# Kernel tuning notes

Hardware: AMD Instinct MI355X
Metric: run time of the kernel (lower is better)

## Reference

```python
import jax, jax.numpy as jnp
import numpy as np

MOMENTUM = 0.1
C_DIM = 5


def setup_inputs() -> dict:
    key = jax.random.key(0)
    k1, k2, k3 = jax.random.split(key, 3)
    B, C, H, W = 16, 256, 128, 128
    im = jax.random.normal(k1, (B, C, H, W), dtype=jnp.float32)
    running_mean = jnp.zeros((2 * C_DIM, C), dtype=jnp.float32)
    running_std = jnp.ones((2 * C_DIM, C), dtype=jnp.float32)
    c_trg = jax.random.randint(k2, (B, C_DIM), 0, 2, dtype=jnp.int32)
    c_org = jax.random.randint(k3, (B, C_DIM), 0, 2, dtype=jnp.int32)
    return {"im": im, "running_mean": running_mean, "running_std": running_std,
            "c_trg": c_trg, "c_org": c_org}


def reference(im, running_mean, running_std, c_trg, c_org):
    B, C, H, W = im.shape
    N = H * W
    # per-sample per-channel instance stats; torch.std_mean uses correction=1
    mean = jnp.mean(im, axis=(2, 3))                      # [B, C]
    var = jnp.sum((im - mean[:, :, None, None]) ** 2, axis=(2, 3)) / (N - 1)
    std = jnp.sqrt(var)                                   # [B, C]

    ct = c_trg.astype(bool)
    co = c_org.astype(bool)
    c_trg_full = jnp.concatenate([ct, ~ct], axis=1)       # [B, 2*c_dim]
    c_org_full = jnp.concatenate([co, ~co], axis=1)       # [B, 2*c_dim]

    m = jnp.float32(MOMENTUM)

    # sequential EMA update of running buffers, in batch order (matches torch loop)
    def step(carry, xs):
        rm, rs = carry
        std_n, mean_n, org_n = xs                         # [C], [C], [2*c_dim]
        msk = org_n[:, None]                              # [2*c_dim, 1]
        rs = jnp.where(msk, rs * (1 - m) + std_n[None, :] * m, rs)
        rm = jnp.where(msk, rm * (1 - m) + mean_n[None, :] * m, rm)
        return (rm, rs), None

    (rm_final, rs_final), _ = jax.lax.scan(
        step, (running_mean, running_std), (std, mean, c_org_full))

    # per-sample gather: mean of selected buffer rows. Exactly c_dim rows are
    # selected per sample (each attribute contributes itself or its negation).
    sel = c_trg_full.astype(im.dtype)                     # [B, 2*c_dim]
    cnt = jnp.sum(sel, axis=1, keepdims=True)             # [B, 1] (== c_dim)
    trg_std = (sel @ rs_final) / cnt                      # [B, C]
    trg_mean = (sel @ rm_final) / cnt                     # [B, C]

    def bc(x):  # [B, C] -> [B, C, 1, 1]
        return x[:, :, None, None]

    return (im - bc(mean)) / bc(std) * bc(trg_std) + bc(trg_mean)
```

## Files before the change

### kernel.cpp

```cpp
#include <hip/hip_runtime.h>
#include <math.h>

#define CDIM 5
constexpr int B_ = 16;
constexpr int C_ = 256;
constexpr int HW_ = 128 * 128;
constexpr float MOM = 0.1f;

using f32x4 = __attribute__((ext_vector_type(4))) float;

__global__ __launch_bounds__(256) void cin_stats(const float* __restrict__ im,
                                                 float* __restrict__ ws_mean,
                                                 float* __restrict__ ws_std) {
    const int plane = blockIdx.x;
    const f32x4* p4 = (const f32x4*)(im + (size_t)plane * HW_);
    const int t = threadIdx.x;

    float sum = 0.f, sumsq = 0.f;
    #pragma unroll
    for (int it = 0; it < 16; ++it) {
        f32x4 v = p4[it * 256 + t];
        sum   += v.x + v.y + v.z + v.w;
        sumsq += v.x * v.x + v.y * v.y + v.z * v.z + v.w * v.w;
    }

    #pragma unroll
    for (int off = 32; off > 0; off >>= 1) {
        sum   += __shfl_down(sum, off, 64);
        sumsq += __shfl_down(sumsq, off, 64);
    }

    __shared__ float s_sum[4], s_sq[4];
    const int wave = t >> 6;
    if ((t & 63) == 0) { s_sum[wave] = sum; s_sq[wave] = sumsq; }
    __syncthreads();

    if (t == 0) {
        float s = s_sum[0] + s_sum[1] + s_sum[2] + s_sum[3];
        float q = s_sq[0] + s_sq[1] + s_sq[2] + s_sq[3];
        float mean = s / (float)HW_;
        float var = fmaxf(q - s * mean, 0.f) / (float)(HW_ - 1);
        ws_mean[plane] = mean;
        ws_std[plane]  = sqrtf(var);
    }
}

__global__ __launch_bounds__(256) void cin_scan(const float* __restrict__ running_mean,
                                                const float* __restrict__ running_std,
                                                const int* __restrict__ c_org,
                                                const float* __restrict__ ws_mean,
                                                const float* __restrict__ ws_std,
                                                float* __restrict__ ws_rm,
                                                float* __restrict__ ws_rs) {
    const int r = blockIdx.x;
    const int c = threadIdx.x;

    float rm = running_mean[r * C_ + c];
    float rs = running_std [r * C_ + c];
    const int k = (r < CDIM) ? r : r - CDIM;

    for (int n = 0; n < B_; ++n) {
        const int bit = c_org[n * CDIM + k];
        const bool msk = (r < CDIM) ? (bit != 0) : (bit == 0);
        if (msk) {
            rs = rs * (1.f - MOM) + ws_std [n * C_ + c] * MOM;
            rm = rm * (1.f - MOM) + ws_mean[n * C_ + c] * MOM;
        }
    }
    ws_rm[r * C_ + c] = rm;
    ws_rs[r * C_ + c] = rs;
}

__global__ __launch_bounds__(256) void cin_norm(const float* __restrict__ im,
                                                const float* __restrict__ ws_mean,
                                                const float* __restrict__ ws_std,
                                                const float* __restrict__ ws_rm,
                                                const float* __restrict__ ws_rs,
                                                const int* __restrict__ c_trg,
                                                float* __restrict__ out) {
    const int plane = (B_ * C_ - 1) - blockIdx.x;
    const int b = plane >> 8;
    const int c = plane & (C_ - 1);

    float tm = 0.f, ts = 0.f, cnt = 0.f;
    #pragma unroll
    for (int r = 0; r < 2 * CDIM; ++r) {
        const int k = (r < CDIM) ? r : r - CDIM;
        const int bit = c_trg[b * CDIM + k];
        const bool sel = (r < CDIM) ? (bit != 0) : (bit == 0);
        if (sel) {
            cnt += 1.f;
            tm  += ws_rm[r * C_ + c];
            ts  += ws_rs[r * C_ + c];
        }
    }
    tm /= cnt;
    ts /= cnt;
    const float mean  = ws_mean[plane];
    const float std   = ws_std [plane];
    const float scale = ts / std;
    const float shift = tm - mean * scale;

    const f32x4* p4 = (const f32x4*)(im + (size_t)plane * HW_);
    f32x4*       o4 = (f32x4*)(out + (size_t)plane * HW_);
    const int t = threadIdx.x;

    #pragma unroll
    for (int it = 0; it < 16; ++it) {
        f32x4 v = p4[it * 256 + t];
        f32x4 r;
        r.x = fmaf(v.x, scale, shift);
        r.y = fmaf(v.y, scale, shift);
        r.z = fmaf(v.z, scale, shift);
        r.w = fmaf(v.w, scale, shift);
        __builtin_nontemporal_store(r, &o4[it * 256 + t]);
    }
}

extern "C" void kernel_launch(void* const* d_in, const int* in_sizes, int n_in,
                              void* d_out, int out_size, void* d_ws, size_t ws_size,
                              hipStream_t stream) {
    const float* im           = (const float*)d_in[0];
    const float* running_mean = (const float*)d_in[1];
    const float* running_std  = (const float*)d_in[2];
    const int*   c_trg        = (const int*)d_in[3];
    const int*   c_org        = (const int*)d_in[4];
    float* out = (float*)d_out;

    float* ws      = (float*)d_ws;
    float* ws_mean = ws;
    float* ws_std  = ws + B_ * C_;
    float* ws_rm   = ws + 2 * B_ * C_;
    float* ws_rs   = ws + 2 * B_ * C_ + 2 * CDIM * C_;

    const int planes = B_ * C_;

    cin_stats<<<planes, 256, 0, stream>>>(im, ws_mean, ws_std);
    cin_scan<<<2 * CDIM, 256, 0, stream>>>(running_mean, running_std, c_org,
                                           ws_mean, ws_std, ws_rm, ws_rs);
    cin_norm<<<planes, 256, 0, stream>>>(im, ws_mean, ws_std, ws_rm, ws_rs,
                                         c_trg, out);
}
```

Before: 128.3 us.

## Stripe channels across launches and fold EMA scan into normalize kernel

The channel dimension is split into four stripes, and each stripe runs its stats and normalize kernels back to back. The working set of one stripe (64 MB) may then stay resident in the large last-level cache for the second read. The separate scan kernel is removed: each normalize block recomputes the sequential EMA over the batch for its channel in registers, which is redundant work across the batch. The change adds more kernel launches (eight instead of three) and per-block scan overhead, in exchange for less HBM re-read traffic.

```diff
diff --git a/kernel.cpp b/kernel.cpp
--- a/kernel.cpp
+++ b/kernel.cpp
@@ -7,12 +7,19 @@
 constexpr int HW_ = 128 * 128;
 constexpr float MOM = 0.1f;
 
+constexpr int NSTRIPES = 4;
+constexpr int CPS = C_ / NSTRIPES;
+
 using f32x4 = __attribute__((ext_vector_type(4))) float;
 
 __global__ __launch_bounds__(256) void cin_stats(const float* __restrict__ im,
                                                  float* __restrict__ ws_mean,
-                                                 float* __restrict__ ws_std) {
-    const int plane = blockIdx.x;
+                                                 float* __restrict__ ws_std,
+                                                 int c0) {
+    const int ci = blockIdx.x % CPS;
+    const int b  = blockIdx.x / CPS;
+    const int plane = b * C_ + c0 + ci;
+
     const f32x4* p4 = (const f32x4*)(im + (size_t)plane * HW_);
     const int t = threadIdx.x;
 
@@ -45,42 +52,42 @@
     }
 }
 
-__global__ __launch_bounds__(256) void cin_scan(const float* __restrict__ running_mean,
+__global__ __launch_bounds__(256) void cin_norm(const float* __restrict__ im,
+                                                const float* __restrict__ running_mean,
                                                 const float* __restrict__ running_std,
+                                                const int* __restrict__ c_trg,
                                                 const int* __restrict__ c_org,
                                                 const float* __restrict__ ws_mean,
                                                 const float* __restrict__ ws_std,
-                                                float* __restrict__ ws_rm,
-                                                float* __restrict__ ws_rs) {
-    const int r = blockIdx.x;
-    const int c = threadIdx.x;
+                                                float* __restrict__ out,
+                                                int c0) {
+    const int ci = blockIdx.x % CPS;
+    const int b  = blockIdx.x / CPS;
+    const int c  = c0 + ci;
+    const int plane = b * C_ + c;
 
-    float rm = running_mean[r * C_ + c];
-    float rs = running_std [r * C_ + c];
-    const int k = (r < CDIM) ? r : r - CDIM;
-
+    float rm[2 * CDIM], rs[2 * CDIM];
+    #pragma unroll
+    for (int r = 0; r < 2 * CDIM; ++r) {
+        rm[r] = running_mean[r * C_ + c];
+        rs[r] = running_std [r * C_ + c];
+    }
     for (int n = 0; n < B_; ++n) {
-        const int bit = c_org[n * CDIM + k];
-        const bool msk = (r < CDIM) ? (bit != 0) : (bit == 0);
-        if (msk) {
-            rs = rs * (1.f - MOM) + ws_std [n * C_ + c] * MOM;
-            rm = rm * (1.f - MOM) + ws_mean[n * C_ + c] * MOM;
+        const float mn = ws_mean[n * C_ + c];
+        const float sd = ws_std [n * C_ + c];
+        int bits[CDIM];
+        #pragma unroll
+        for (int k = 0; k < CDIM; ++k) bits[k] = c_org[n * CDIM + k];
+        #pragma unroll
+        for (int r = 0; r < 2 * CDIM; ++r) {
+            const int k = (r < CDIM) ? r : r - CDIM;
+            const bool msk = (r < CDIM) ? (bits[k] != 0) : (bits[k] == 0);
+            if (msk) {
+                rs[r] = rs[r] * (1.f - MOM) + sd * MOM;
+                rm[r] = rm[r] * (1.f - MOM) + mn * MOM;
+            }
         }
     }
-    ws_rm[r * C_ + c] = rm;
-    ws_rs[r * C_ + c] = rs;
-}
-
-__global__ __launch_bounds__(256) void cin_norm(const float* __restrict__ im,
-                                                const float* __restrict__ ws_mean,
-                                                const float* __restrict__ ws_std,
-                                                const float* __restrict__ ws_rm,
-                                                const float* __restrict__ ws_rs,
-                                                const int* __restrict__ c_trg,
-                                                float* __restrict__ out) {
-    const int plane = (B_ * C_ - 1) - blockIdx.x;
-    const int b = plane >> 8;
-    const int c = plane & (C_ - 1);
 
     float tm = 0.f, ts = 0.f, cnt = 0.f;
     #pragma unroll
@@ -88,11 +95,7 @@
         const int k = (r < CDIM) ? r : r - CDIM;
         const int bit = c_trg[b * CDIM + k];
         const bool sel = (r < CDIM) ? (bit != 0) : (bit == 0);
-        if (sel) {
-            cnt += 1.f;
-            tm  += ws_rm[r * C_ + c];
-            ts  += ws_rs[r * C_ + c];
-        }
+        if (sel) { cnt += 1.f; tm += rm[r]; ts += rs[r]; }
     }
     tm /= cnt;
     ts /= cnt;
@@ -130,14 +133,14 @@
     float* ws      = (float*)d_ws;
     float* ws_mean = ws;
     float* ws_std  = ws + B_ * C_;
-    float* ws_rm   = ws + 2 * B_ * C_;
-    float* ws_rs   = ws + 2 * B_ * C_ + 2 * CDIM * C_;
 
-    const int planes = B_ * C_;
+    const int blocks = B_ * CPS;
 
-    cin_stats<<<planes, 256, 0, stream>>>(im, ws_mean, ws_std);
-    cin_scan<<<2 * CDIM, 256, 0, stream>>>(running_mean, running_std, c_org,
-                                           ws_mean, ws_std, ws_rm, ws_rs);
-    cin_norm<<<planes, 256, 0, stream>>>(im, ws_mean, ws_std, ws_rm, ws_rs,
-                                         c_trg, out);
+    for (int s = 0; s < NSTRIPES; ++s) {
+        const int c0 = s * CPS;
+        cin_stats<<<blocks, 256, 0, stream>>>(im, ws_mean, ws_std, c0);
+        cin_norm <<<blocks, 256, 0, stream>>>(im, running_mean, running_std,
+                                              c_trg, c_org, ws_mean, ws_std,
+                                              out, c0);
+    }
 }
```

Result: slower. 149.3 us (+16.4%).
